# Kernel optimization log

Hardware: AMD Instinct MI355X
Metric: run time of the kernel (lower is better)

## Reference

```python
import jax, jax.numpy as jnp
import numpy as np


def setup_inputs() -> dict:
    key = jax.random.key(0)
    k1, k2 = jax.random.split(key)
    enc_output = jax.random.normal(k1, (4, 4096, 1024), dtype=jnp.float32)
    dec_output = jax.random.normal(k2, (4, 4096, 1024), dtype=jnp.float32)
    return {"enc_output": enc_output, "dec_output": dec_output}


def reference(enc_output, dec_output):
    # a_t[b, e, t] = sum_d enc[b, e, d] * dec[b, t, d]   -> [B, T_enc, T_dec]
    a_t = jnp.einsum('bed,btd->bet', enc_output, dec_output)
    # softmax over dim=1 (the T_enc axis), no scaling, no mask (faithful to source)
    a_t = jax.nn.softmax(a_t, axis=1)
    # c_t[b, t, d] = sum_e a_t[b, e, t] * enc[b, e, d]   -> [B, T_dec, D]
    c_t = jnp.einsum('bet,bed->btd', a_t, enc_output)
    return c_t
```

## Files before the change

kernel.cpp:

```cpp
#include <hip/hip_runtime.h>
#include <hip/hip_fp16.h>

typedef _Float16 half_t;
typedef _Float16 f16x8 __attribute__((ext_vector_type(8)));
typedef _Float16 f16x4 __attribute__((ext_vector_type(4)));
typedef float f32x4 __attribute__((ext_vector_type(4)));

#define SEQ 4096
#define DDIM 1024
#define NBATCH 4

__device__ __forceinline__ void gload16(const half_t* g, half_t* l) {
  __builtin_amdgcn_global_load_lds((const __attribute__((address_space(1))) void*)g,
                                   (__attribute__((address_space(3))) void*)l, 16, 0, 0);
}

__global__ __launch_bounds__(256) void conv_f16(const float* __restrict__ src,
                                                half_t* __restrict__ dst) {
  int i = blockIdx.x * 256 + threadIdx.x;
  float4 x = ((const float4*)src)[i];
  f16x4 o = {(half_t)x.x, (half_t)x.y, (half_t)x.z, (half_t)x.w};
  *(f16x4*)(dst + (size_t)i * 4) = o;
}

__global__ __launch_bounds__(256) void transpose_f16(const float* __restrict__ src,
                                                     half_t* __restrict__ dst) {
  __shared__ float tile[32][33];
  int b = blockIdx.z;
  int e0 = blockIdx.x * 32, d0 = blockIdx.y * 32;
  const float* s = src + (size_t)b * SEQ * DDIM;
  half_t* dt = dst + (size_t)b * DDIM * SEQ;
  int tx = threadIdx.x & 31, ty = threadIdx.x >> 5;
#pragma unroll
  for (int i = 0; i < 4; i++) {
    int e = e0 + ty + i * 8;
    tile[ty + i * 8][tx] = s[(size_t)e * DDIM + d0 + tx];
  }
  __syncthreads();
#pragma unroll
  for (int i = 0; i < 4; i++) {
    int d = d0 + ty + i * 8;
    dt[(size_t)d * SEQ + e0 + tx] = (half_t)tile[tx][ty + i * 8];
  }
}

#define BM 128
#define BN 128
#define BK 64

__global__ __launch_bounds__(256) void gemm_f16(const half_t* __restrict__ A,
                                                const half_t* __restrict__ B,
                                                float* __restrict__ C, int M, int N, int K,
                                                int kc, long sA, long sB, long sC, int atom) {
  A += (size_t)blockIdx.z * (size_t)sA;
  B += (size_t)blockIdx.z * (size_t)sB;
  C += (size_t)blockIdx.z * (size_t)sC;
  __shared__ __align__(16) half_t As[BM * BK];
  __shared__ __align__(16) half_t Bs[BN * BK];
  const int tid = threadIdx.x;
  const int bm = blockIdx.x, bn = blockIdx.y;
  const int wave = tid >> 6, lane = tid & 63;
  const int wm = (wave & 1) * 64, wn = (wave >> 1) * 64;
  const int mrow = lane & 15, quad = lane >> 4;

  f32x4 acc[4][4];
#pragma unroll
  for (int i = 0; i < 4; i++)
#pragma unroll
    for (int j = 0; j < 4; j++) acc[i][j] = {0.f, 0.f, 0.f, 0.f};

  const half_t* Ag = A + (size_t)(bm * BM) * K;
  const half_t* Bg = B + (size_t)(bn * BN) * K;

  for (int k0 = 0; k0 < kc; k0 += BK) {
#pragma unroll
    for (int i = 0; i < 4; i++) {
      int cid = i * 256 + tid;
      int row = cid >> 3, slot = cid & 7;
      int chunk = slot ^ (row & 7);
      gload16(Ag + (size_t)row * K + k0 + chunk * 8, &As[row * BK + slot * 8]);
      gload16(Bg + (size_t)row * K + k0 + chunk * 8, &Bs[row * BK + slot * 8]);
    }
    __builtin_amdgcn_s_waitcnt(0);
    __syncthreads();
#pragma unroll
    for (int ks = 0; ks < 2; ks++) {
      f16x8 af[4], bf[4];
#pragma unroll
      for (int i = 0; i < 4; i++) {
        int ra = wm + i * 16 + mrow;
        int rb = wn + i * 16 + mrow;
        int sa = (ks * 4 + quad) ^ (ra & 7);
        int sb = (ks * 4 + quad) ^ (rb & 7);
        af[i] = *(const f16x8*)(&As[ra * BK + sa * 8]);
        bf[i] = *(const f16x8*)(&Bs[rb * BK + sb * 8]);
      }
#pragma unroll
      for (int mi = 0; mi < 4; mi++)
#pragma unroll
        for (int ni = 0; ni < 4; ni++)
          acc[mi][ni] =
              __builtin_amdgcn_mfma_f32_16x16x32_f16(af[mi], bf[ni], acc[mi][ni], 0, 0, 0);
    }
    __syncthreads();
  }
#pragma unroll
  for (int mi = 0; mi < 4; mi++) {
#pragma unroll
    for (int ni = 0; ni < 4; ni++) {
      int row0 = bm * BM + wm + mi * 16 + quad * 4;
      int col = bn * BN + wn + ni * 16 + mrow;
      float* Cp = C + (size_t)row0 * N + col;
      if (atom) {
#pragma unroll
        for (int r = 0; r < 4; r++) unsafeAtomicAdd(Cp + (size_t)r * N, acc[mi][ni][r]);
      } else {
#pragma unroll
        for (int r = 0; r < 4; r++) Cp[(size_t)r * N] = acc[mi][ni][r];
      }
    }
  }
}

__global__ __launch_bounds__(256) void softmax_rows(const float* __restrict__ S,
                                                    half_t* __restrict__ P) {
  const int row = blockIdx.x;
  const float4* Sr = (const float4*)(S + (size_t)row * SEQ);
  const int tid = threadIdx.x, lane = tid & 63, wave = tid >> 6;
  __shared__ float red[4];
  __shared__ float bc;
  float4 v[4];
  float m = -1e30f;
#pragma unroll
  for (int j = 0; j < 4; j++) {
    v[j] = Sr[tid + j * 256];
    m = fmaxf(m, fmaxf(fmaxf(v[j].x, v[j].y), fmaxf(v[j].z, v[j].w)));
  }
#pragma unroll
  for (int o = 32; o; o >>= 1) m = fmaxf(m, __shfl_xor(m, o));
  if (lane == 0) red[wave] = m;
  __syncthreads();
  if (tid == 0) bc = fmaxf(fmaxf(red[0], red[1]), fmaxf(red[2], red[3]));
  __syncthreads();
  m = bc;
  float s = 0.f;
#pragma unroll
  for (int j = 0; j < 4; j++) {
    v[j].x = __expf(v[j].x - m);
    v[j].y = __expf(v[j].y - m);
    v[j].z = __expf(v[j].z - m);
    v[j].w = __expf(v[j].w - m);
    s += v[j].x + v[j].y + v[j].z + v[j].w;
  }
#pragma unroll
  for (int o = 32; o; o >>= 1) s += __shfl_xor(s, o);
  __syncthreads();
  if (lane == 0) red[wave] = s;
  __syncthreads();
  if (tid == 0) bc = red[0] + red[1] + red[2] + red[3];
  __syncthreads();
  float r = 1.0f / bc;
  f16x4* Pr = (f16x4*)(P + (size_t)row * SEQ);
#pragma unroll
  for (int j = 0; j < 4; j++) {
    f16x4 o = {(half_t)(v[j].x * r), (half_t)(v[j].y * r), (half_t)(v[j].z * r),
               (half_t)(v[j].w * r)};
    Pr[tid + j * 256] = o;
  }
}

__global__ __launch_bounds__(256) void naive_attn(const float* __restrict__ enc,
                                                  const float* __restrict__ dec,
                                                  float* __restrict__ out) {
  const int b = blockIdx.y, t = blockIdx.x;
  const float* encb = enc + (size_t)b * SEQ * DDIM;
  const float* q = dec + ((size_t)b * SEQ + t) * DDIM;
  __shared__ float qs[DDIM];
  __shared__ float sc[SEQ];
  __shared__ float red[4];
  __shared__ float bc;
  const int tid = threadIdx.x, lane = tid & 63, wave = tid >> 6;
  for (int i = tid; i < DDIM; i += 256) qs[i] = q[i];
  __syncthreads();
  for (int e = tid; e < SEQ; e += 256) {
    const float* er = encb + (size_t)e * DDIM;
    float s = 0.f;
    for (int d = 0; d < DDIM; d += 4) {
      float4 ev = *(const float4*)(er + d);
      s += ev.x * qs[d] + ev.y * qs[d + 1] + ev.z * qs[d + 2] + ev.w * qs[d + 3];
    }
    sc[e] = s;
  }
  __syncthreads();
  float m = -1e30f;
  for (int e = tid; e < SEQ; e += 256) m = fmaxf(m, sc[e]);
#pragma unroll
  for (int o = 32; o; o >>= 1) m = fmaxf(m, __shfl_xor(m, o));
  if (lane == 0) red[wave] = m;
  __syncthreads();
  if (tid == 0) bc = fmaxf(fmaxf(red[0], red[1]), fmaxf(red[2], red[3]));
  __syncthreads();
  m = bc;
  float s = 0.f;
  for (int e = tid; e < SEQ; e += 256) {
    float p = __expf(sc[e] - m);
    sc[e] = p;
    s += p;
  }
#pragma unroll
  for (int o = 32; o; o >>= 1) s += __shfl_xor(s, o);
  __syncthreads();
  if (lane == 0) red[wave] = s;
  __syncthreads();
  if (tid == 0) bc = red[0] + red[1] + red[2] + red[3];
  __syncthreads();
  const float rinv = 1.0f / bc;
  const int d0 = tid * 4;
  float4 acc = {0.f, 0.f, 0.f, 0.f};
  for (int e = 0; e < SEQ; e++) {
    float p = sc[e];
    float4 ev = *(const float4*)(encb + (size_t)e * DDIM + d0);
    acc.x += p * ev.x;
    acc.y += p * ev.y;
    acc.z += p * ev.z;
    acc.w += p * ev.w;
  }
  float4* o4 = (float4*)(out + ((size_t)b * SEQ + t) * DDIM + d0);
  float4 res = {acc.x * rinv, acc.y * rinv, acc.z * rinv, acc.w * rinv};
  *o4 = res;
}

extern "C" void kernel_launch(void* const* d_in, const int* in_sizes, int n_in, void* d_out,
                              int out_size, void* d_ws, size_t ws_size, hipStream_t stream) {
  const float* enc = (const float*)d_in[0];
  const float* dec = (const float*)d_in[1];
  float* out = (float*)d_out;

  const size_t SZ_S = (size_t)SEQ * SEQ * 4;
  const size_t SZ_P = (size_t)SEQ * SEQ * 2;
  const size_t SZ_PALL = (size_t)NBATCH * SEQ * SEQ * 2;
  const size_t SZ_H = (size_t)NBATCH * SEQ * DDIM * 2;
  const size_t NEED_SPLITK = SZ_S + SZ_P + 3 * SZ_H;
  const size_t NEED_BATCH = SZ_S + SZ_PALL + 3 * SZ_H;

  const int nconv = NBATCH * SEQ * DDIM / 4 / 256;

  if (ws_size >= NEED_BATCH) {
    char* w = (char*)d_ws;
    float* S = (float*)w;
    half_t* Pall = (half_t*)(w + SZ_S);
    half_t* decF = (half_t*)(w + SZ_S + SZ_PALL);
    half_t* encF = (half_t*)(w + SZ_S + SZ_PALL + SZ_H);
    half_t* encT = (half_t*)(w + SZ_S + SZ_PALL + 2 * SZ_H);

    conv_f16<<<nconv, 256, 0, stream>>>(dec, decF);
    conv_f16<<<nconv, 256, 0, stream>>>(enc, encF);
    transpose_f16<<<dim3(SEQ / 32, DDIM / 32, NBATCH), 256, 0, stream>>>(enc, encT);

    for (int b = 0; b < NBATCH; b++) {
      const size_t eo = (size_t)b * SEQ * DDIM;
      gemm_f16<<<dim3(SEQ / BM, SEQ / BN, 1), 256, 0, stream>>>(decF + eo, encF + eo, S, SEQ,
                                                                SEQ, DDIM, DDIM, 0, 0, 0, 0);
      softmax_rows<<<SEQ, 256, 0, stream>>>(S, Pall + (size_t)b * SEQ * SEQ);
    }
    gemm_f16<<<dim3(SEQ / BM, DDIM / BN, NBATCH), 256, 0, stream>>>(
        Pall, encT, out, SEQ, DDIM, SEQ, SEQ, (long)SEQ * SEQ, (long)DDIM * SEQ,
        (long)SEQ * DDIM, 0);
  } else if (ws_size >= NEED_SPLITK) {
    char* w = (char*)d_ws;
    float* S = (float*)w;
    half_t* P = (half_t*)(w + SZ_S);
    half_t* decF = (half_t*)(w + SZ_S + SZ_P);
    half_t* encF = (half_t*)(w + SZ_S + SZ_P + SZ_H);
    half_t* encT = (half_t*)(w + SZ_S + SZ_P + 2 * SZ_H);

    hipMemsetAsync(out, 0, (size_t)NBATCH * SEQ * DDIM * 4, stream);
    conv_f16<<<nconv, 256, 0, stream>>>(dec, decF);
    conv_f16<<<nconv, 256, 0, stream>>>(enc, encF);
    transpose_f16<<<dim3(SEQ / 32, DDIM / 32, NBATCH), 256, 0, stream>>>(enc, encT);

    for (int b = 0; b < NBATCH; b++) {
      const size_t eo = (size_t)b * SEQ * DDIM;
      gemm_f16<<<dim3(SEQ / BM, SEQ / BN, 1), 256, 0, stream>>>(decF + eo, encF + eo, S, SEQ,
                                                                SEQ, DDIM, DDIM, 0, 0, 0, 0);
      softmax_rows<<<SEQ, 256, 0, stream>>>(S, P);
      gemm_f16<<<dim3(SEQ / BM, DDIM / BN, 4), 256, 0, stream>>>(
          P, encT + (size_t)b * DDIM * SEQ, out + eo, SEQ, DDIM, SEQ, SEQ / 4, SEQ / 4,
          SEQ / 4, 0, 1);
    }
  } else {
    naive_attn<<<dim3(SEQ, NBATCH), 256, 0, stream>>>(enc, dec, out);
  }
}
```

Baseline: 823.3 us.

## Double-buffer GEMM LDS tiles, fuse enc convert/transpose, batch all GEMMs

The GEMM kernel now ping-pongs two LDS buffers, issuing async global-to-LDS loads for the next K tile while computing on the current one, and drops the explicit full waitcnt before each tile. The enc fp16 conversion is merged into the transpose kernel so enc is read once. A new path, used when the workspace is large enough, runs the score GEMM and softmax for all batches in single launches. The trade-off is more LDS use per block, which may lower occupancy, and a possible ordering hazard if the async loads are not waited on before use.

```diff
diff --git a/kernel.cpp b/kernel.cpp
--- a/kernel.cpp
+++ b/kernel.cpp
@@ -23,18 +23,22 @@
   *(f16x4*)(dst + (size_t)i * 4) = o;
 }
 
-__global__ __launch_bounds__(256) void transpose_f16(const float* __restrict__ src,
-                                                     half_t* __restrict__ dst) {
+__global__ __launch_bounds__(256) void transconv_f16(const float* __restrict__ src,
+                                                     half_t* __restrict__ dstF,
+                                                     half_t* __restrict__ dstT) {
   __shared__ float tile[32][33];
   int b = blockIdx.z;
   int e0 = blockIdx.x * 32, d0 = blockIdx.y * 32;
   const float* s = src + (size_t)b * SEQ * DDIM;
-  half_t* dt = dst + (size_t)b * DDIM * SEQ;
+  half_t* df = dstF + (size_t)b * SEQ * DDIM;
+  half_t* dt = dstT + (size_t)b * DDIM * SEQ;
   int tx = threadIdx.x & 31, ty = threadIdx.x >> 5;
 #pragma unroll
   for (int i = 0; i < 4; i++) {
     int e = e0 + ty + i * 8;
-    tile[ty + i * 8][tx] = s[(size_t)e * DDIM + d0 + tx];
+    float v = s[(size_t)e * DDIM + d0 + tx];
+    tile[ty + i * 8][tx] = v;
+    df[(size_t)e * DDIM + d0 + tx] = (half_t)v;
   }
   __syncthreads();
 #pragma unroll
@@ -55,8 +59,8 @@
   A += (size_t)blockIdx.z * (size_t)sA;
   B += (size_t)blockIdx.z * (size_t)sB;
   C += (size_t)blockIdx.z * (size_t)sC;
-  __shared__ __align__(16) half_t As[BM * BK];
-  __shared__ __align__(16) half_t Bs[BN * BK];
+  __shared__ __align__(16) half_t As[2][BM * BK];
+  __shared__ __align__(16) half_t Bs[2][BN * BK];
   const int tid = threadIdx.x;
   const int bm = blockIdx.x, bn = blockIdx.y;
   const int wave = tid >> 6, lane = tid & 63;
@@ -72,17 +76,22 @@
   const half_t* Ag = A + (size_t)(bm * BM) * K;
   const half_t* Bg = B + (size_t)(bn * BN) * K;
 
-  for (int k0 = 0; k0 < kc; k0 += BK) {
+  auto stage = [&](int buf, int k0) {
 #pragma unroll
     for (int i = 0; i < 4; i++) {
       int cid = i * 256 + tid;
       int row = cid >> 3, slot = cid & 7;
       int chunk = slot ^ (row & 7);
-      gload16(Ag + (size_t)row * K + k0 + chunk * 8, &As[row * BK + slot * 8]);
-      gload16(Bg + (size_t)row * K + k0 + chunk * 8, &Bs[row * BK + slot * 8]);
-    }
-    __builtin_amdgcn_s_waitcnt(0);
-    __syncthreads();
+      gload16(Ag + (size_t)row * K + k0 + chunk * 8, &As[buf][row * BK + slot * 8]);
+      gload16(Bg + (size_t)row * K + k0 + chunk * 8, &Bs[buf][row * BK + slot * 8]);
+    }
+  };
+
+  stage(0, 0);
+  __syncthreads();
+  int cur = 0;
+  for (int k0 = 0; k0 < kc; k0 += BK) {
+    if (k0 + BK < kc) stage(cur ^ 1, k0 + BK);
 #pragma unroll
     for (int ks = 0; ks < 2; ks++) {
       f16x8 af[4], bf[4];
@@ -92,8 +101,8 @@
         int rb = wn + i * 16 + mrow;
         int sa = (ks * 4 + quad) ^ (ra & 7);
         int sb = (ks * 4 + quad) ^ (rb & 7);
-        af[i] = *(const f16x8*)(&As[ra * BK + sa * 8]);
-        bf[i] = *(const f16x8*)(&Bs[rb * BK + sb * 8]);
+        af[i] = *(const f16x8*)(&As[cur][ra * BK + sa * 8]);
+        bf[i] = *(const f16x8*)(&Bs[cur][rb * BK + sb * 8]);
       }
 #pragma unroll
       for (int mi = 0; mi < 4; mi++)
@@ -103,6 +112,7 @@
               __builtin_amdgcn_mfma_f32_16x16x32_f16(af[mi], bf[ni], acc[mi][ni], 0, 0, 0);
     }
     __syncthreads();
+    cur ^= 1;
   }
 #pragma unroll
   for (int mi = 0; mi < 4; mi++) {
@@ -237,15 +247,34 @@
   float* out = (float*)d_out;
 
   const size_t SZ_S = (size_t)SEQ * SEQ * 4;
+  const size_t SZ_SALL = (size_t)NBATCH * SEQ * SEQ * 4;
   const size_t SZ_P = (size_t)SEQ * SEQ * 2;
   const size_t SZ_PALL = (size_t)NBATCH * SEQ * SEQ * 2;
   const size_t SZ_H = (size_t)NBATCH * SEQ * DDIM * 2;
+  const size_t NEED_FULL = SZ_SALL + SZ_PALL + 3 * SZ_H;
+  const size_t NEED_BATCH = SZ_S + SZ_PALL + 3 * SZ_H;
   const size_t NEED_SPLITK = SZ_S + SZ_P + 3 * SZ_H;
-  const size_t NEED_BATCH = SZ_S + SZ_PALL + 3 * SZ_H;
 
   const int nconv = NBATCH * SEQ * DDIM / 4 / 256;
 
-  if (ws_size >= NEED_BATCH) {
+  if (ws_size >= NEED_FULL) {
+    char* w = (char*)d_ws;
+    float* Sall = (float*)w;
+    half_t* Pall = (half_t*)(w + SZ_SALL);
+    half_t* decF = (half_t*)(w + SZ_SALL + SZ_PALL);
+    half_t* encF = (half_t*)(w + SZ_SALL + SZ_PALL + SZ_H);
+    half_t* encT = (half_t*)(w + SZ_SALL + SZ_PALL + 2 * SZ_H);
+
+    conv_f16<<<nconv, 256, 0, stream>>>(dec, decF);
+    transconv_f16<<<dim3(SEQ / 32, DDIM / 32, NBATCH), 256, 0, stream>>>(enc, encF, encT);
+    gemm_f16<<<dim3(SEQ / BM, SEQ / BN, NBATCH), 256, 0, stream>>>(
+        decF, encF, Sall, SEQ, SEQ, DDIM, DDIM, (long)SEQ * DDIM, (long)SEQ * DDIM,
+        (long)SEQ * SEQ, 0);
+    softmax_rows<<<NBATCH * SEQ, 256, 0, stream>>>(Sall, Pall);
+    gemm_f16<<<dim3(SEQ / BM, DDIM / BN, NBATCH), 256, 0, stream>>>(
+        Pall, encT, out, SEQ, DDIM, SEQ, SEQ, (long)SEQ * SEQ, (long)DDIM * SEQ,
+        (long)SEQ * DDIM, 0);
+  } else if (ws_size >= NEED_BATCH) {
     char* w = (char*)d_ws;
     float* S = (float*)w;
     half_t* Pall = (half_t*)(w + SZ_S);
@@ -254,8 +283,7 @@
     half_t* encT = (half_t*)(w + SZ_S + SZ_PALL + 2 * SZ_H);
 
     conv_f16<<<nconv, 256, 0, stream>>>(dec, decF);
-    conv_f16<<<nconv, 256, 0, stream>>>(enc, encF);
-    transpose_f16<<<dim3(SEQ / 32, DDIM / 32, NBATCH), 256, 0, stream>>>(enc, encT);
+    transconv_f16<<<dim3(SEQ / 32, DDIM / 32, NBATCH), 256, 0, stream>>>(enc, encF, encT);
 
     for (int b = 0; b < NBATCH; b++) {
       const size_t eo = (size_t)b * SEQ * DDIM;
@@ -276,8 +304,7 @@
 
     hipMemsetAsync(out, 0, (size_t)NBATCH * SEQ * DDIM * 4, stream);
     conv_f16<<<nconv, 256, 0, stream>>>(dec, decF);
-    conv_f16<<<nconv, 256, 0, stream>>>(enc, encF);
-    transpose_f16<<<dim3(SEQ / 32, DDIM / 32, NBATCH), 256, 0, stream>>>(enc, encT);
+    transconv_f16<<<dim3(SEQ / 32, DDIM / 32, NBATCH), 256, 0, stream>>>(enc, encF, encT);
 
     for (int b = 0; b < NBATCH; b++) {
       const size_t eo = (size_t)b * SEQ * DDIM;
```

After: 749.1 us. 9.0% less time.
